# Optimization experiments

Measured on AMD Instinct MI355X. Metric: run time of the kernel, lower is better.

The kernel has to match this reference:

```python
import jax, jax.numpy as jnp
import numpy as np

# Multi-scale feature pyramid (H, W) per level, standard Deformable-DETR for ~800x800 input
SHAPES = [(100, 100), (50, 50), (25, 25), (13, 13)]
D = 256      # d_model
NH = 8       # n_heads
NL = 4       # n_levels
NP = 4       # n_points
HD = D // NH # head_dim = 32
B = 2
S = sum(h * w for h, w in SHAPES)  # 13294
Lq = S  # encoder-style: one query per multi-scale token


def setup_inputs() -> dict:
    key = jax.random.key(0)
    ks = jax.random.split(key, 11)
    return {
        "query": jax.random.normal(ks[0], (B, Lq, D), jnp.float32),
        "reference_points": jax.random.uniform(ks[1], (B, Lq, NL, 2), jnp.float32),
        "value": jax.random.normal(ks[2], (B, S, D), jnp.float32),
        "W_val": jax.random.normal(ks[3], (D, D), jnp.float32) * 0.02,
        "b_val": jnp.zeros((D,), jnp.float32),
        "W_off": jax.random.normal(ks[4], (D, NH * NL * NP * 2), jnp.float32) * 0.01,
        "b_off": jax.random.normal(ks[5], (NH * NL * NP * 2,), jnp.float32) * 0.5,
        "W_attn": jax.random.normal(ks[6], (D, NH * NL * NP), jnp.float32) * 0.02,
        "b_attn": jnp.zeros((NH * NL * NP,), jnp.float32),
        "W_out": jax.random.normal(ks[7], (D, D), jnp.float32) * 0.02,
        "b_out": jnp.zeros((D,), jnp.float32),
    }


def _bilinear_sample(valf, x, y, H, W):
    """grid_sample(mode=bilinear, padding_mode=zeros, align_corners=False).
    valf: [N, H*W, C] flattened feature map; x, y: [N, P] pixel-space coords
    (already converted via x = loc_x*W - 0.5). Returns [N, P, C].
    """
    x0 = jnp.floor(x); y0 = jnp.floor(y)
    x1 = x0 + 1.0;     y1 = y0 + 1.0
    wx1 = x - x0; wx0 = 1.0 - wx1
    wy1 = y - y0; wy0 = 1.0 - wy1

    def corner(xi, yi, w):
        inb = (xi >= 0) & (xi <= W - 1) & (yi >= 0) & (yi <= H - 1)
        xi_c = jnp.clip(xi, 0, W - 1).astype(jnp.int32)
        yi_c = jnp.clip(yi, 0, H - 1).astype(jnp.int32)
        idx = yi_c * W + xi_c                                   # [N, P]
        v = jnp.take_along_axis(valf, idx[..., None], axis=1)   # [N, P, C]
        return v * (w * inb.astype(valf.dtype))[..., None]

    return (corner(x0, y0, wx0 * wy0) + corner(x1, y0, wx1 * wy0)
            + corner(x0, y1, wx0 * wy1) + corner(x1, y1, wx1 * wy1))


def reference(query, reference_points, value, W_val, b_val, W_off, b_off,
              W_attn, b_attn, W_out, b_out):
    Bq, L, _ = query.shape
    # value projection, split into heads: [B, S, NH, HD]
    val = (value @ W_val + b_val).reshape(Bq, S, NH, HD)
    # sampling offsets and attention weights from query
    offsets = (query @ W_off + b_off).reshape(Bq, L, NH, NL, NP, 2)
    w = (query @ W_attn + b_attn).reshape(Bq, L, NH, NL * NP)
    w = jax.nn.softmax(w, axis=-1).reshape(Bq, L, NH, NL, NP)
    # normalize offsets by (W, H) per level; 2D reference points path
    offset_norm = jnp.array([[wd, h] for h, wd in SHAPES], jnp.float32)  # [NL, 2]
    locs = (reference_points[:, :, None, :, None, :]
            + offsets / offset_norm[None, None, None, :, None, :])       # [B,L,NH,NL,NP,2]

    splits = [h * wd for h, wd in SHAPES]
    starts = np.concatenate([[0], np.cumsum(splits)])
    out_acc = jnp.zeros((Bq, L, NH, HD), query.dtype)
    for lvl, (H, W) in enumerate(SHAPES):
        vl = val[:, starts[lvl]:starts[lvl + 1]]                 # [B, HW, NH, HD]
        vl = vl.transpose(0, 2, 1, 3).reshape(Bq * NH, H * W, HD)
        loc = locs[:, :, :, lvl].transpose(0, 2, 1, 3, 4).reshape(Bq * NH, L * NP, 2)
        x = loc[..., 0] * W - 0.5   # align_corners=False pixel coords
        y = loc[..., 1] * H - 0.5
        s = _bilinear_sample(vl, x, y, H, W).reshape(Bq, NH, L, NP, HD)
        wl = w[:, :, :, lvl].transpose(0, 2, 1, 3)               # [B, NH, L, NP]
        out_acc = out_acc + jnp.einsum('bhqpd,bhqp->bqhd', s, wl)
    out = out_acc.reshape(Bq, L, NH * HD)
    return out @ W_out + b_out
```

## Files before the change

kernel.cpp:

```cpp
#include <hip/hip_runtime.h>
#include <hip/hip_bf16.h>
#include <math.h>

#define B_    2
#define NH_   8
#define NL_   4
#define NP_   4
#define HD_   32
#define S_    13294
#define L_    13294
#define M_    26588

__device__ __constant__ int c_H[NL_]     = {100, 50, 25, 13};
__device__ __constant__ int c_W[NL_]     = {100, 50, 25, 13};
__device__ __constant__ int c_start[NL_] = {0, 10000, 12500, 13125};

typedef __attribute__((ext_vector_type(8))) _Float16 f16x8;
typedef __attribute__((ext_vector_type(2))) _Float16 f16x2;
typedef __attribute__((ext_vector_type(4))) float    float4v;

__device__ __forceinline__ unsigned short f2h(float f) {
    _Float16 h = (_Float16)f;
    return __builtin_bit_cast(unsigned short, h);
}
__device__ __forceinline__ float h2f(unsigned short u) {
    _Float16 h = __builtin_bit_cast(_Float16, u);
    return (float)h;
}
__device__ __forceinline__ f16x2 pkrtz(float a, float b) {
    return __builtin_bit_cast(f16x2, __builtin_amdgcn_cvt_pkrtz(a, b));
}

__global__ __launch_bounds__(256) void prep_weights(
    const float* __restrict__ W_val, const float* __restrict__ W_off,
    const float* __restrict__ W_attn, const float* __restrict__ b_off,
    const float* __restrict__ b_attn, const float* __restrict__ W_out,
    unsigned short* __restrict__ wt_val, unsigned short* __restrict__ wt_oa,
    unsigned short* __restrict__ wt_out, float* __restrict__ bias_oa)
{
    int i = blockIdx.x * 256 + threadIdx.x;
    if (i < 65536) {
        int n = i >> 8, k = i & 255;
        wt_val[i] = f2h(W_val[k * 256 + n]);
    } else if (i < 65536 + 98304) {
        int j = i - 65536;
        int n = j >> 8, k = j & 255;
        float v = (n < 256) ? W_off[k * 256 + n] : W_attn[k * 128 + (n - 256)];
        wt_oa[j] = f2h(v);
    } else if (i < 65536 + 98304 + 65536) {
        int j = i - 163840;
        int n = j >> 8, k = j & 255;
        wt_out[j] = f2h(W_out[k * 256 + n]);
    } else if (i < 229376 + 384) {
        int j = i - 229376;
        bias_oa[j] = (j < 256) ? b_off[j] : b_attn[j - 256];
    }
}

template<int N, int OUT, bool AF32>
__device__ __forceinline__ void gemm_body(
    const void* __restrict__ Av,
    const unsigned short* __restrict__ WT,
    const float* __restrict__ bias,
    void* __restrict__ Cv,
    unsigned short (* __restrict__ As)[64][40])
{
    constexpr int NT = N / 64;

    const int tid  = threadIdx.x;
    const int lane = tid & 63;
    const int wave = tid >> 6;
    const int rowBase = blockIdx.x * 64;
    const int wcol = wave * (N / 4);

    const int ar   = tid >> 2;
    const int ako  = (tid & 3) * 8;
    const int grow = rowBase + ar;
    const int fr   = lane & 15;
    const int fk   = (lane >> 4) * 8;

    float4v acc[4][NT] = {};

    const unsigned short* bbase[NT];
#pragma unroll
    for (int t = 0; t < NT; ++t)
        bbase[t] = WT + (size_t)(wcol + t * 16 + fr) * 256 + fk;

    f16x8 curB[NT], nxtB[NT];
    float4 ra0, ra1;
    f16x8  rah;

    auto loadA = [&](int k0) {
        if constexpr (AF32) {
            const float* A = (const float*)Av;
            if (grow < M_) {
                ra0 = *reinterpret_cast<const float4*>(A + (size_t)grow * 256 + k0 + ako);
                ra1 = *reinterpret_cast<const float4*>(A + (size_t)grow * 256 + k0 + ako + 4);
            } else { ra0 = make_float4(0.f,0.f,0.f,0.f); ra1 = ra0; }
        } else {
            const unsigned short* A = (const unsigned short*)Av;
            if (grow < M_)
                rah = *reinterpret_cast<const f16x8*>(A + (size_t)grow * 256 + k0 + ako);
            else
                rah = f16x8{};
        }
    };
    auto storeA = [&](int buf) {
        f16x8 s;
        if constexpr (AF32) {
            f16x2 p0 = pkrtz(ra0.x, ra0.y);
            f16x2 p1 = pkrtz(ra0.z, ra0.w);
            f16x2 p2 = pkrtz(ra1.x, ra1.y);
            f16x2 p3 = pkrtz(ra1.z, ra1.w);
            s[0]=p0[0]; s[1]=p0[1]; s[2]=p1[0]; s[3]=p1[1];
            s[4]=p2[0]; s[5]=p2[1]; s[6]=p3[0]; s[7]=p3[1];
        } else {
            s = rah;
        }
        *reinterpret_cast<f16x8*>(&As[buf][ar][ako]) = s;
    };
    auto loadB = [&](f16x8* dst, int k0) {
#pragma unroll
        for (int t = 0; t < NT; ++t)
            dst[t] = *reinterpret_cast<const f16x8*>(bbase[t] + k0);
    };

    loadA(0);
    loadB(curB, 0);
    storeA(0);
    loadA(32);

#pragma unroll
    for (int it = 0; it < 8; ++it) {
        __syncthreads();
        f16x8 af[4];
#pragma unroll
        for (int t = 0; t < 4; ++t)
            af[t] = *reinterpret_cast<const f16x8*>(&As[it & 1][t * 16 + fr][fk]);
        if (it < 7) {
            storeA((it + 1) & 1);
            if (it < 6) loadA((it + 2) * 32);
            loadB(nxtB, (it + 1) * 32);
        }
#pragma unroll
        for (int mt = 0; mt < 4; ++mt)
#pragma unroll
            for (int nt = 0; nt < NT; ++nt)
                acc[mt][nt] = __builtin_amdgcn_mfma_f32_16x16x32_f16(
                    af[mt], curB[nt], acc[mt][nt], 0, 0, 0);
        if (it < 7) {
#pragma unroll
            for (int t = 0; t < NT; ++t) curB[t] = nxtB[t];
        }
    }

    const int dn  = lane & 15;
    const int dm0 = (lane >> 4) * 4;
#pragma unroll
    for (int mt = 0; mt < 4; ++mt) {
#pragma unroll
        for (int nt = 0; nt < NT; ++nt) {
            const int col = wcol + nt * 16 + dn;
            const float bv = bias[col];
#pragma unroll
            for (int r = 0; r < 4; ++r) {
                const int row = rowBase + mt * 16 + dm0 + r;
                if (row < M_) {
                    const float v = acc[mt][nt][r] + bv;
                    if constexpr (OUT == 0)
                        ((unsigned short*)Cv)[(size_t)row * 256 + col] = f2h(v);
                    else if constexpr (OUT == 1)
                        ((unsigned short*)Cv)[(size_t)row * 384 + col] = f2h(v);
                    else
                        ((float*)Cv)[(size_t)row * 256 + col] = v;
                }
            }
        }
    }
}

__global__ __launch_bounds__(256) void gemm_vq(
    const float* __restrict__ value, const float* __restrict__ query,
    const unsigned short* __restrict__ wt_val, const unsigned short* __restrict__ wt_oa,
    const float* __restrict__ b_val, const float* __restrict__ bias_oa,
    unsigned short* __restrict__ val_f16, unsigned short* __restrict__ oa_f16)
{
    __shared__ unsigned short As[2][64][40];
    if (blockIdx.y == 0)
        gemm_body<256, 0, true>(value, wt_val, b_val, val_f16, As);
    else
        gemm_body<384, 1, true>(query, wt_oa, bias_oa, oa_f16, As);
}

__global__ __launch_bounds__(256) void gemm_out3(
    const unsigned short* __restrict__ Af16,
    const unsigned short* __restrict__ WT,
    const float* __restrict__ bias, float* __restrict__ C)
{
    __shared__ unsigned short As[2][64][40];
    gemm_body<256, 2, false>(Af16, WT, bias, C, As);
}

__global__ __launch_bounds__(256) void deform_sample_v5(
    const unsigned short* __restrict__ val,
    const float* __restrict__ refp,
    const unsigned short* __restrict__ oa,
    unsigned short* __restrict__ acc)
{
    const int tid = threadIdx.x;
    const int q0  = blockIdx.x * 8;

    __shared__ unsigned short sLog[8][128];
    __shared__ float sMS[8][8][2];
    __shared__ int   sPack[8][4][16][8];

    {
        const int q  = tid >> 5;
        const int f  = tid & 31;
        const int bq = min(q0 + q, M_ - 1);
        *reinterpret_cast<int2*>(&sLog[q][f * 4]) =
            *reinterpret_cast<const int2*>(oa + (size_t)bq * 384 + 256 + f * 4);
    }
    __syncthreads();

    if (tid < 64) {
        const int q = tid >> 3, h = tid & 7;
        float m = -1e30f;
#pragma unroll
        for (int i = 0; i < 16; ++i) m = fmaxf(m, h2f(sLog[q][h * 16 + i]));
        float s = 0.f;
#pragma unroll
        for (int i = 0; i < 16; ++i) s += __expf(h2f(sLog[q][h * 16 + i]) - m);
        sMS[q][h][0] = m;
        sMS[q][h][1] = 1.f / s;
    }
    __syncthreads();

#pragma unroll
    for (int k = 0; k < 4; ++k) {
        const int e   = tid + k * 256;
        const int q   = e >> 7;
        const int t   = e & 127;
        const int h   = t >> 4;
        const int lp  = t & 15;
        const int lvl = lp >> 2;
        const int p   = lp & 3;
        const int bq  = min(q0 + q, M_ - 1);

        const float wgt = __expf(h2f(sLog[q][t]) - sMS[q][h][0]) * sMS[q][h][1];

        const int Wi = c_W[lvl], Hi = c_H[lvl], st = c_start[lvl];
        const float rx = refp[((size_t)bq * NL_ + lvl) * 2 + 0];
        const float ry = refp[((size_t)bq * NL_ + lvl) * 2 + 1];
        const float ox = h2f(oa[(size_t)bq * 384 + h * 32 + lvl * 8 + p * 2 + 0]);
        const float oy = h2f(oa[(size_t)bq * 384 + h * 32 + lvl * 8 + p * 2 + 1]);
        const float x = rx * (float)Wi + ox - 0.5f;
        const float y = ry * (float)Hi + oy - 0.5f;

        const float x0f = floorf(x), y0f = floorf(y);
        const int   x0 = (int)x0f,   y0 = (int)y0f;
        const float wx1 = x - x0f, wx0 = 1.f - wx1;
        const float wy1 = y - y0f, wy0 = 1.f - wy1;

        const int   cx[4] = {x0, x0 + 1, x0,     x0 + 1};
        const int   cy[4] = {y0, y0,     y0 + 1, y0 + 1};
        const float cw[4] = {wx0 * wy0, wx1 * wy0, wx0 * wy1, wx1 * wy1};
#pragma unroll
        for (int c = 0; c < 4; ++c) {
            const bool inb = (cx[c] >= 0) & (cx[c] < Wi) & (cy[c] >= 0) & (cy[c] < Hi);
            const int xi = min(max(cx[c], 0), Wi - 1);
            const int yi = min(max(cy[c], 0), Hi - 1);
            const int idx = st + yi * Wi + xi;
            const unsigned short wh = f2h(inb ? wgt * cw[c] : 0.f);
            sPack[q][c][lp][h] = idx | ((int)wh << 16);
        }
    }
    __syncthreads();

    const int q  = tid >> 5;
    const int h  = (tid >> 2) & 7;
    const int d4 = tid & 3;
    const int bq = q0 + q;
    const int b  = min(bq, M_ - 1) / L_;
    const unsigned short* vb = val + (size_t)b * S_ * 256 + h * 32 + d4 * 8;

    f16x2 A0{}, A1{}, A2{}, A3{};
#pragma unroll 8
    for (int i = 0; i < 64; ++i) {
        const int lp = i >> 2;
        const int c  = i & 3;
        const int pk = sPack[q][c][lp][h];
        const unsigned wb = (unsigned)pk >> 16;
        const f16x2 w2 = __builtin_bit_cast(f16x2, (wb << 16) | wb);
        const int4 u = *reinterpret_cast<const int4*>(
            vb + (size_t)((unsigned)pk & 0xffffu) * 256);
        A0 += w2 * __builtin_bit_cast(f16x2, u.x);
        A1 += w2 * __builtin_bit_cast(f16x2, u.y);
        A2 += w2 * __builtin_bit_cast(f16x2, u.z);
        A3 += w2 * __builtin_bit_cast(f16x2, u.w);
    }
    if (bq < M_) {
        int4 o;
        o.x = __builtin_bit_cast(int, A0);
        o.y = __builtin_bit_cast(int, A1);
        o.z = __builtin_bit_cast(int, A2);
        o.w = __builtin_bit_cast(int, A3);
        *reinterpret_cast<int4*>(acc + (size_t)bq * 256 + h * 32 + d4 * 8) = o;
    }
}

extern "C" void kernel_launch(void* const* d_in, const int* in_sizes, int n_in,
                              void* d_out, int out_size, void* d_ws, size_t ws_size,
                              hipStream_t stream) {
    const float* query  = (const float*)d_in[0];
    const float* refp   = (const float*)d_in[1];
    const float* value  = (const float*)d_in[2];
    const float* W_val  = (const float*)d_in[3];
    const float* b_val  = (const float*)d_in[4];
    const float* W_off  = (const float*)d_in[5];
    const float* b_off  = (const float*)d_in[6];
    const float* W_attn = (const float*)d_in[7];
    const float* b_attn = (const float*)d_in[8];
    const float* W_out  = (const float*)d_in[9];
    const float* b_out  = (const float*)d_in[10];
    float* out = (float*)d_out;

    char* ws = (char*)d_ws;
    const size_t mb = (size_t)M_ * 256;
    unsigned short* val_f16 = (unsigned short*)ws;  ws += mb * 2;
    unsigned short* acc_f16 = (unsigned short*)ws;  ws += mb * 2;
    unsigned short* oa_f16  = (unsigned short*)ws;  ws += (size_t)M_ * 384 * 2;
    unsigned short* wt_val  = (unsigned short*)ws;  ws += 65536 * 2;
    unsigned short* wt_oa   = (unsigned short*)ws;  ws += 98304 * 2;
    unsigned short* wt_out  = (unsigned short*)ws;  ws += 65536 * 2;
    float*          bias_oa = (float*)ws;           ws += 384 * 4;

    dim3 blk(256);

    prep_weights<<<dim3(898), blk, 0, stream>>>(
        W_val, W_off, W_attn, b_off, b_attn, W_out, wt_val, wt_oa, wt_out, bias_oa);

    gemm_vq<<<dim3((M_ + 63) / 64, 2), blk, 0, stream>>>(
        value, query, wt_val, wt_oa, b_val, bias_oa, val_f16, oa_f16);

    deform_sample_v5<<<dim3((M_ + 7) / 8), blk, 0, stream>>>(val_f16, refp, oa_f16, acc_f16);

    gemm_out3<<<dim3((M_ + 63) / 64), blk, 0, stream>>>(acc_f16, wt_out, b_out, out);
}
```

Before: 210.5 us.

## Restructure deformable sampling per wave with shuffle softmax and no block barriers

Each 64-lane wave now handles two queries end to end. Every lane loads four logits and does the softmax with lane shuffles across the four levels of a head, then computes the packed index/weight entries for its level's four points. Those entries go into a per-wave padded LDS region, so all three __syncthreads are gone, and the launch bounds ask for higher occupancy. The trade is less parallelism in the prep phase, since each thread now handles four points instead of one element per loop step, plus padding to cut LDS bank conflicts.

```diff
diff --git a/kernel.cpp b/kernel.cpp
--- a/kernel.cpp
+++ b/kernel.cpp
@@ -201,95 +201,86 @@
     gemm_body<256, 2, false>(Af16, WT, bias, C, As);
 }
 
-__global__ __launch_bounds__(256) void deform_sample_v5(
+__global__ __launch_bounds__(256, 8) void deform_sample_v6(
     const unsigned short* __restrict__ val,
     const float* __restrict__ refp,
     const unsigned short* __restrict__ oa,
     unsigned short* __restrict__ acc)
 {
-    const int tid = threadIdx.x;
-    const int q0  = blockIdx.x * 8;
-
-    __shared__ unsigned short sLog[8][128];
-    __shared__ float sMS[8][8][2];
-    __shared__ int   sPack[8][4][16][8];
+    __shared__ int sP[4][1088];
+
+    const int tid  = threadIdx.x;
+    const int wave = tid >> 6;
+    const int l    = tid & 63;
+
+    const int q   = l >> 5;
+    const int h   = (l >> 2) & 7;
+    const int lvl = l & 3;
+    const int qw  = blockIdx.x * 8 + wave * 2 + q;
+    const int bq  = min(qw, M_ - 1);
+
+    int* __restrict__ sw = sP[wave];
 
     {
-        const int q  = tid >> 5;
-        const int f  = tid & 31;
-        const int bq = min(q0 + q, M_ - 1);
-        *reinterpret_cast<int2*>(&sLog[q][f * 4]) =
-            *reinterpret_cast<const int2*>(oa + (size_t)bq * 384 + 256 + f * 4);
-    }
-    __syncthreads();
-
-    if (tid < 64) {
-        const int q = tid >> 3, h = tid & 7;
-        float m = -1e30f;
-#pragma unroll
-        for (int i = 0; i < 16; ++i) m = fmaxf(m, h2f(sLog[q][h * 16 + i]));
-        float s = 0.f;
-#pragma unroll
-        for (int i = 0; i < 16; ++i) s += __expf(h2f(sLog[q][h * 16 + i]) - m);
-        sMS[q][h][0] = m;
-        sMS[q][h][1] = 1.f / s;
-    }
-    __syncthreads();
-
-#pragma unroll
-    for (int k = 0; k < 4; ++k) {
-        const int e   = tid + k * 256;
-        const int q   = e >> 7;
-        const int t   = e & 127;
-        const int h   = t >> 4;
-        const int lp  = t & 15;
-        const int lvl = lp >> 2;
-        const int p   = lp & 3;
-        const int bq  = min(q0 + q, M_ - 1);
-
-        const float wgt = __expf(h2f(sLog[q][t]) - sMS[q][h][0]) * sMS[q][h][1];
+        const int2 lgi = *reinterpret_cast<const int2*>(
+            oa + (size_t)bq * 384 + 256 + h * 16 + lvl * 4);
+        const f16x2 lp0 = __builtin_bit_cast(f16x2, lgi.x);
+        const f16x2 lp1 = __builtin_bit_cast(f16x2, lgi.y);
+        float lg[4] = { (float)lp0[0], (float)lp0[1], (float)lp1[0], (float)lp1[1] };
+
+        float m = fmaxf(fmaxf(lg[0], lg[1]), fmaxf(lg[2], lg[3]));
+        m = fmaxf(m, __shfl_xor(m, 1));
+        m = fmaxf(m, __shfl_xor(m, 2));
+
+        float e[4], s = 0.f;
+#pragma unroll
+        for (int j = 0; j < 4; ++j) { e[j] = __expf(lg[j] - m); s += e[j]; }
+        s += __shfl_xor(s, 1);
+        s += __shfl_xor(s, 2);
+        const float rinv = 1.f / s;
 
         const int Wi = c_W[lvl], Hi = c_H[lvl], st = c_start[lvl];
-        const float rx = refp[((size_t)bq * NL_ + lvl) * 2 + 0];
-        const float ry = refp[((size_t)bq * NL_ + lvl) * 2 + 1];
-        const float ox = h2f(oa[(size_t)bq * 384 + h * 32 + lvl * 8 + p * 2 + 0]);
-        const float oy = h2f(oa[(size_t)bq * 384 + h * 32 + lvl * 8 + p * 2 + 1]);
-        const float x = rx * (float)Wi + ox - 0.5f;
-        const float y = ry * (float)Hi + oy - 0.5f;
-
-        const float x0f = floorf(x), y0f = floorf(y);
-        const int   x0 = (int)x0f,   y0 = (int)y0f;
-        const float wx1 = x - x0f, wx0 = 1.f - wx1;
-        const float wy1 = y - y0f, wy0 = 1.f - wy1;
-
-        const int   cx[4] = {x0, x0 + 1, x0,     x0 + 1};
-        const int   cy[4] = {y0, y0,     y0 + 1, y0 + 1};
-        const float cw[4] = {wx0 * wy0, wx1 * wy0, wx0 * wy1, wx1 * wy1};
-#pragma unroll
-        for (int c = 0; c < 4; ++c) {
-            const bool inb = (cx[c] >= 0) & (cx[c] < Wi) & (cy[c] >= 0) & (cy[c] < Hi);
-            const int xi = min(max(cx[c], 0), Wi - 1);
-            const int yi = min(max(cy[c], 0), Hi - 1);
-            const int idx = st + yi * Wi + xi;
-            const unsigned short wh = f2h(inb ? wgt * cw[c] : 0.f);
-            sPack[q][c][lp][h] = idx | ((int)wh << 16);
-        }
-    }
-    __syncthreads();
-
-    const int q  = tid >> 5;
-    const int h  = (tid >> 2) & 7;
-    const int d4 = tid & 3;
-    const int bq = q0 + q;
-    const int b  = min(bq, M_ - 1) / L_;
-    const unsigned short* vb = val + (size_t)b * S_ * 256 + h * 32 + d4 * 8;
+        const float2 rxy = *reinterpret_cast<const float2*>(
+            refp + ((size_t)bq * NL_ + lvl) * 2);
+        const f16x8 off8 = *reinterpret_cast<const f16x8*>(
+            oa + (size_t)bq * 384 + h * 32 + lvl * 8);
+
+#pragma unroll
+        for (int j = 0; j < 4; ++j) {
+            const float wgt = e[j] * rinv;
+            const float x = rxy.x * (float)Wi + (float)off8[2 * j]     - 0.5f;
+            const float y = rxy.y * (float)Hi + (float)off8[2 * j + 1] - 0.5f;
+            const float x0f = floorf(x), y0f = floorf(y);
+            const int   x0 = (int)x0f,   y0 = (int)y0f;
+            const float wx1 = x - x0f, wx0 = 1.f - wx1;
+            const float wy1 = y - y0f, wy0 = 1.f - wy1;
+
+            const int   cx[4] = {x0, x0 + 1, x0,     x0 + 1};
+            const int   cy[4] = {y0, y0,     y0 + 1, y0 + 1};
+            const float cw[4] = {wx0 * wy0, wx1 * wy0, wx0 * wy1, wx1 * wy1};
+            const int base = q * 544 + (lvl * 4 + j) * 34 + h;
+#pragma unroll
+            for (int c = 0; c < 4; ++c) {
+                const bool inb = (cx[c] >= 0) & (cx[c] < Wi) & (cy[c] >= 0) & (cy[c] < Hi);
+                const int xi = min(max(cx[c], 0), Wi - 1);
+                const int yi = min(max(cy[c], 0), Hi - 1);
+                const int idx = st + yi * Wi + xi;
+                const unsigned short wh = f2h(inb ? wgt * cw[c] : 0.f);
+                sw[base + c * 8] = idx | ((int)wh << 16);
+            }
+        }
+    }
+
+    const int d4 = lvl;
+    const unsigned short* vb = val + (size_t)(bq / L_) * S_ * 256 + h * 32 + d4 * 8;
+    const int rbase = q * 544 + h;
 
     f16x2 A0{}, A1{}, A2{}, A3{};
 #pragma unroll 8
     for (int i = 0; i < 64; ++i) {
         const int lp = i >> 2;
         const int c  = i & 3;
-        const int pk = sPack[q][c][lp][h];
+        const int pk = sw[rbase + lp * 34 + c * 8];
         const unsigned wb = (unsigned)pk >> 16;
         const f16x2 w2 = __builtin_bit_cast(f16x2, (wb << 16) | wb);
         const int4 u = *reinterpret_cast<const int4*>(
@@ -299,13 +290,13 @@
         A2 += w2 * __builtin_bit_cast(f16x2, u.z);
         A3 += w2 * __builtin_bit_cast(f16x2, u.w);
     }
-    if (bq < M_) {
+    if (qw < M_) {
         int4 o;
         o.x = __builtin_bit_cast(int, A0);
         o.y = __builtin_bit_cast(int, A1);
         o.z = __builtin_bit_cast(int, A2);
         o.w = __builtin_bit_cast(int, A3);
-        *reinterpret_cast<int4*>(acc + (size_t)bq * 256 + h * 32 + d4 * 8) = o;
+        *reinterpret_cast<int4*>(acc + (size_t)qw * 256 + h * 32 + d4 * 8) = o;
     }
 }
 
@@ -343,7 +334,7 @@
     gemm_vq<<<dim3((M_ + 63) / 64, 2), blk, 0, stream>>>(
         value, query, wt_val, wt_oa, b_val, bias_oa, val_f16, oa_f16);
 
-    deform_sample_v5<<<dim3((M_ + 7) / 8), blk, 0, stream>>>(val_f16, refp, oa_f16, acc_f16);
+    deform_sample_v6<<<dim3((M_ + 7) / 8), blk, 0, stream>>>(val_f16, refp, oa_f16, acc_f16);
 
     gemm_out3<<<dim3((M_ + 63) / 64), blk, 0, stream>>>(acc_f16, wt_out, b_out, out);
 }
```

New measurement: 208.7 us. Within noise of the previous version (-0.8%).
